# Kernel optimization log

Measured on AMD Instinct MI355X. Metric: run time of the kernel, lower is better.

Reference implementation:

```python
import jax, jax.numpy as jnp
import numpy as np

B, S, D = 2, 2048, 1024
H = 16
DH = D // H
FFN = 4096
EPS = 1e-5
SCALE = 1.0 / np.sqrt(DH).astype(np.float32)


def layer_norm(x, g, b):
    mu = jnp.mean(x, axis=-1, keepdims=True)
    var = jnp.mean(jnp.square(x - mu), axis=-1, keepdims=True)
    return (x - mu) * jax.lax.rsqrt(var + EPS) * g + b


def setup_inputs() -> dict:
    key = jax.random.key(0)
    ks = jax.random.split(key, 12)
    std = 0.02
    return {
        "x": jax.random.normal(ks[0], (B, S, D), dtype=jnp.float32),
        "mask": jax.random.randint(ks[1], (B, S), 0, 2, dtype=jnp.int32),
        "w_qkv": jax.random.normal(ks[2], (D, 3 * D), dtype=jnp.float32) * std,
        "w_out": jax.random.normal(ks[3], (D, D), dtype=jnp.float32) * std,
        "b_out": jnp.zeros((D,), dtype=jnp.float32),
        "g1": jnp.ones((D,), dtype=jnp.float32),
        "be1": jnp.zeros((D,), dtype=jnp.float32),
        "g2": jnp.ones((D,), dtype=jnp.float32),
        "be2": jnp.zeros((D,), dtype=jnp.float32),
        "w1": jax.random.normal(ks[4], (D, FFN), dtype=jnp.float32) * std,
        "b1": jnp.zeros((FFN,), dtype=jnp.float32),
        "w2": jax.random.normal(ks[5], (FFN, D), dtype=jnp.float32) * std,
        "b2": jnp.zeros((D,), dtype=jnp.float32),
    }


def reference(x, mask, w_qkv, w_out, b_out, g1, be1, g2, be2, w1, b1, w2, b2):
    # --- pre-norm self-attention ---
    h = layer_norm(x, g1, be1)                              # [B,S,D]
    qkv = (h @ w_qkv).reshape(B, S, 3, H, DH)               # [B,S,3,H,Dh]
    q, k, v = [jnp.transpose(qkv[:, :, i], (0, 2, 1, 3)) for i in range(3)]  # [B,H,S,Dh]
    scores = jnp.einsum("bhqd,bhkd->bhqk", q, k) * SCALE    # [B,H,S,S]
    key_mask = (mask != 0)[:, None, None, :]                # [B,1,1,S]
    scores = jnp.where(key_mask, scores, -1e9)
    attn = jax.nn.softmax(scores, axis=-1)
    out = jnp.einsum("bhqk,bhkd->bhqd", attn, v)            # [B,H,S,Dh]
    out = jnp.transpose(out, (0, 2, 1, 3)).reshape(B, S, D)
    x = x + (out @ w_out + b_out)
    # --- pre-norm FFN ---
    h2 = layer_norm(x, g2, be2)
    ffn = jax.nn.relu(h2 @ w1 + b1) @ w2 + b2
    return x + ffn
```

## Files before the change

### kernel.cpp

```cpp
#include <hip/hip_runtime.h>

typedef unsigned short u16;
typedef __bf16 bf16x8 __attribute__((ext_vector_type(8)));
typedef float f32x4 __attribute__((ext_vector_type(4)));

typedef __attribute__((address_space(1))) const void* as1cv;
typedef __attribute__((address_space(3))) void* as3v;

__device__ __forceinline__ u16 f2bf(float f) {
  union { float f; unsigned u; } v;
  v.f = f;
  unsigned r = (v.u + 0x7fffu + ((v.u >> 16) & 1u)) >> 16;
  return (u16)r;
}

__device__ __forceinline__ unsigned cvtpk(float lo, float hi) {
  unsigned r;
  asm("v_cvt_pk_bf16_f32 %0, %1, %2" : "=v"(r) : "v"(lo), "v"(hi));
  return r;
}

__device__ __forceinline__ void gload16(const void* g, void* l) {
  __builtin_amdgcn_global_load_lds((as1cv)g, (as3v)l, 16, 0, 0);
}

__global__ __launch_bounds__(256)
void ln_kernel(const float* __restrict__ x, const float* __restrict__ g,
               const float* __restrict__ be, u16* __restrict__ out) {
  __shared__ float red[8];
  const int row = blockIdx.x;
  const int tid = threadIdx.x;
  const float4 v = ((const float4*)(x + (size_t)row * 1024))[tid];
  float s = v.x + v.y + v.z + v.w;
#pragma unroll
  for (int off = 1; off < 64; off <<= 1) s += __shfl_xor(s, off, 64);
  const int wv = tid >> 6, lane = tid & 63;
  if (lane == 0) red[wv] = s;
  __syncthreads();
  s = red[0] + red[1] + red[2] + red[3];
  const float mu = s * (1.0f / 1024.0f);
  const float d0 = v.x - mu, d1 = v.y - mu, d2 = v.z - mu, d3 = v.w - mu;
  float q = d0 * d0 + d1 * d1 + d2 * d2 + d3 * d3;
#pragma unroll
  for (int off = 1; off < 64; off <<= 1) q += __shfl_xor(q, off, 64);
  if (lane == 0) red[4 + wv] = q;
  __syncthreads();
  q = red[4] + red[5] + red[6] + red[7];
  const float inv = rsqrtf(q * (1.0f / 1024.0f) + 1e-5f);
  const float4 gv = ((const float4*)g)[tid];
  const float4 bv = ((const float4*)be)[tid];
  unsigned p0 = (unsigned)f2bf(d0 * inv * gv.x + bv.x) |
                ((unsigned)f2bf(d1 * inv * gv.y + bv.y) << 16);
  unsigned p1 = (unsigned)f2bf(d2 * inv * gv.z + bv.z) |
                ((unsigned)f2bf(d3 * inv * gv.w + bv.w) << 16);
  uint2 o; o.x = p0; o.y = p1;
  *(uint2*)(out + (size_t)row * 1024 + tid * 4) = o;
}

__global__ __launch_bounds__(256)
void transpose_all(const float* __restrict__ i0, u16* __restrict__ o0,
                   const float* __restrict__ i1, u16* __restrict__ o1,
                   const float* __restrict__ i2, u16* __restrict__ o2,
                   const float* __restrict__ i3, u16* __restrict__ o3) {
  __shared__ float t[32][33];
  int id = blockIdx.x;
  const float* in; u16* out; int K, N, nx;
  if (id < 3072)      { in = i0; out = o0; K = 1024; N = 3072; nx = 96; }
  else if (id < 4096) { id -= 3072; in = i1; out = o1; K = 1024; N = 1024; nx = 32; }
  else if (id < 8192) { id -= 4096; in = i2; out = o2; K = 1024; N = 4096; nx = 128; }
  else                { id -= 8192; in = i3; out = o3; K = 4096; N = 1024; nx = 32; }
  const int n0 = (id % nx) * 32, k0 = (id / nx) * 32;
  const int tx = threadIdx.x & 31, ty = threadIdx.x >> 5;
  for (int r = ty; r < 32; r += 8)
    t[r][tx] = in[(size_t)(k0 + r) * N + n0 + tx];
  __syncthreads();
  for (int r = ty; r < 32; r += 8)
    out[(size_t)(n0 + r) * K + k0 + tx] = f2bf(t[tx][r]);
}

template<int BIAS, int RELU, int RES, int MODE, int NSPLIT>
__global__ __launch_bounds__(256, 2)
void gemm_bt(const u16* __restrict__ A, const u16* __restrict__ Bt,
             const float* __restrict__ bias, const float* __restrict__ res,
             void* __restrict__ C, u16* __restrict__ vt,
             int M, int N, int K, int kChunk) {
  __shared__ u16 As[4][4096];
  __shared__ u16 Bs[4][4096];
  const int tid = threadIdx.x;
  const int wv = tid >> 6, lane = tid & 63;
  const int z = (NSPLIT > 1) ? (int)(blockIdx.x % NSPLIT) : 0;
  const int bm = (int)(blockIdx.x / NSPLIT) * 128;
  const int bn = blockIdx.y * 128;
  const int wr = wv >> 1, wc = wv & 1;
  const int l16 = lane & 15, lh = lane >> 4;

  const int ssk = ((lane & 3) ^ ((lane >> 3) & 3)) << 3;
  const int rdk = (lh ^ ((l16 >> 1) & 3)) << 3;

  f32x4 acc[4][4] = {};

  const int kb = z * kChunk;
  const u16* Ag = A + (size_t)(bm + wv * 16 + (lane >> 2)) * K + kb + ssk;
  const u16* Bg = Bt + (size_t)(bn + wv * 16 + (lane >> 2)) * K + kb + ssk;

#define STG_A(buf, ko)  do { \
    gload16(Ag + (ko), &As[buf][wv * 512]); \
    gload16(Ag + (size_t)64 * K + (ko), &As[buf][2048 + wv * 512]); } while (0)
#define STG_B(buf, ko)  do { \
    gload16(Bg + (ko), &Bs[buf][wv * 512]); \
    gload16(Bg + (size_t)64 * K + (ko), &Bs[buf][2048 + wv * 512]); } while (0)

  const int nst = kChunk >> 5;
  STG_A(0, 0); STG_B(0, 0);
  if (nst > 1) { STG_A(1, 32); STG_B(1, 32); }
  if (nst > 2) { STG_A(2, 64); STG_B(2, 64); }

  for (int t = 0; t < nst; ++t) {
    const int cur = t & 3;
    const int rem = nst - t;
    if (rem >= 3)      asm volatile("s_waitcnt vmcnt(8)" ::: "memory");
    else if (rem == 2) asm volatile("s_waitcnt vmcnt(4)" ::: "memory");
    else               asm volatile("s_waitcnt vmcnt(0)" ::: "memory");
    __builtin_amdgcn_s_barrier();
    asm volatile("" ::: "memory");
    const int nxb = (t + 3) & 3;
    bf16x8 af[4], bfv[4];
#pragma unroll
    for (int i = 0; i < 4; i++)
      af[i] = *(const bf16x8*)&As[cur][(wr * 64 + i * 16 + l16) * 32 + rdk];
#pragma unroll
    for (int j = 0; j < 2; j++)
      bfv[j] = *(const bf16x8*)&Bs[cur][(wc * 64 + j * 16 + l16) * 32 + rdk];
    if (t + 3 < nst) STG_A(nxb, (t + 3) * 32);
    __builtin_amdgcn_s_setprio(1);
#pragma unroll
    for (int i = 0; i < 4; i++)
#pragma unroll
      for (int j = 0; j < 2; j++)
        acc[i][j] = __builtin_amdgcn_mfma_f32_16x16x32_bf16(af[i], bfv[j], acc[i][j], 0, 0, 0);
    __builtin_amdgcn_s_setprio(0);
#pragma unroll
    for (int j = 2; j < 4; j++)
      bfv[j] = *(const bf16x8*)&Bs[cur][(wc * 64 + j * 16 + l16) * 32 + rdk];
    if (t + 3 < nst) STG_B(nxb, (t + 3) * 32);
    __builtin_amdgcn_s_setprio(1);
#pragma unroll
    for (int i = 0; i < 4; i++)
#pragma unroll
      for (int j = 2; j < 4; j++)
        acc[i][j] = __builtin_amdgcn_mfma_f32_16x16x32_bf16(af[i], bfv[j], acc[i][j], 0, 0, 0);
    __builtin_amdgcn_s_setprio(0);
  }
#undef STG_A
#undef STG_B

#pragma unroll
  for (int i = 0; i < 4; i++) {
#pragma unroll
    for (int j = 0; j < 4; j++) {
      const int col = bn + wc * 64 + j * 16 + l16;
      const float bv = (BIAS && z == 0) ? bias[col] : 0.0f;
      if (MODE == 3 && bn >= 2048) {
        const int cc = col - 2048, h = cc >> 6, d = cc & 63;
        const int row0 = bm + wr * 64 + i * 16 + (lane >> 4) * 4;
        const int bb = row0 >> 11, kv0 = row0 & 2047;
        const int p0 = (kv0 & 32) | (((kv0 >> 2) & 3) << 3) | (((kv0 >> 4) & 1) << 2);
        uint2 o;
        o.x = (unsigned)f2bf(acc[i][j][0]) | ((unsigned)f2bf(acc[i][j][1]) << 16);
        o.y = (unsigned)f2bf(acc[i][j][2]) | ((unsigned)f2bf(acc[i][j][3]) << 16);
        *(uint2*)(vt + ((size_t)(bb * 16 + h) * 64 + d) * 2048 + (kv0 & ~63) + p0) = o;
      } else {
#pragma unroll
        for (int r = 0; r < 4; r++) {
          const int row = bm + wr * 64 + i * 16 + (lane >> 4) * 4 + r;
          float v = acc[i][j][r] + bv;
          if (RELU) v = fmaxf(v, 0.0f);
          if (RES) v += res[(size_t)row * N + col];
          if (MODE == 2)       atomicAdd((float*)C + (size_t)row * N + col, v);
          else if (MODE == 0)  ((float*)C)[(size_t)row * N + col] = v;
          else                 ((u16*)C)[(size_t)row * N + col] = f2bf(v);
        }
      }
    }
  }
}

template<int BIAS, int RELU, int MODE>
__global__ __launch_bounds__(512, 2)
void gemm256(const u16* __restrict__ A, const u16* __restrict__ Bt,
             const float* __restrict__ bias, u16* __restrict__ C,
             u16* __restrict__ vt, int M, int N, int K) {
  __shared__ u16 As[2][16384];
  __shared__ u16 Bs[2][16384];
  const int tid = threadIdx.x;
  const int wv = tid >> 6, lane = tid & 63;
  const int l16 = lane & 15, lh = lane >> 4;
  const int wm = wv >> 2, wn = wv & 3;
  const int bm = blockIdx.x * 256, bn = blockIdx.y * 256;

  const int koff = ((lane & 7) ^ ((lane >> 3) & 7)) << 3;
  const int ka0 = ((lh ^ (l16 & 7)) << 3);
  const int ka1 = (((4 + lh) ^ (l16 & 7)) << 3);

  f32x4 acc[8][4] = {};

  const u16* Ag = A + (size_t)(bm + wv * 8 + (lane >> 3)) * K + koff;
  const u16* Bg = Bt + (size_t)(bn + wv * 8 + (lane >> 3)) * K + koff;

#define STAGE256(buf, ko)                                                  \
  do {                                                                     \
    _Pragma("unroll")                                                      \
    for (int j = 0; j < 4; ++j) {                                          \
      gload16(Ag + (size_t)(j * 64) * K + (ko), &As[buf][j * 4096 + wv * 512]); \
      gload16(Bg + (size_t)(j * 64) * K + (ko), &Bs[buf][j * 4096 + wv * 512]); \
    }                                                                      \
  } while (0)

  const int nt = K >> 6;
  STAGE256(0, 0);
  if (nt > 1) STAGE256(1, 64);

  for (int t = 0; t < nt; ++t) {
    const int cur = t & 1;
    if (t + 1 < nt) asm volatile("s_waitcnt vmcnt(8)" ::: "memory");
    else            asm volatile("s_waitcnt vmcnt(0)" ::: "memory");
    __builtin_amdgcn_s_barrier();
    asm volatile("" ::: "memory");
#pragma unroll
    for (int kk = 0; kk < 2; ++kk) {
      const int ko = kk ? ka1 : ka0;
      bf16x8 af[8], bfv[4];
#pragma unroll
      for (int i = 0; i < 8; ++i)
        af[i] = *(const bf16x8*)&As[cur][(wm * 128 + i * 16 + l16) * 64 + ko];
#pragma unroll
      for (int n = 0; n < 4; ++n)
        bfv[n] = *(const bf16x8*)&Bs[cur][(wn * 64 + n * 16 + l16) * 64 + ko];
      __builtin_amdgcn_s_setprio(1);
#pragma unroll
      for (int i = 0; i < 8; ++i)
#pragma unroll
        for (int n = 0; n < 4; ++n)
          acc[i][n] = __builtin_amdgcn_mfma_f32_16x16x32_bf16(af[i], bfv[n], acc[i][n], 0, 0, 0);
      __builtin_amdgcn_s_setprio(0);
    }
    asm volatile("" ::: "memory");
    __builtin_amdgcn_s_barrier();
    asm volatile("" ::: "memory");
    if (t + 2 < nt) STAGE256(cur, (t + 2) * 64);
  }
#undef STAGE256

#pragma unroll
  for (int i = 0; i < 8; ++i)
#pragma unroll
    for (int n = 0; n < 4; ++n) {
      const int col = bn + wn * 64 + n * 16 + l16;
      const float bv = BIAS ? bias[col] : 0.0f;
      if (MODE == 3 && bn >= 2048) {
        const int cc = col - 2048, h = cc >> 6, d = cc & 63;
        const int row0 = bm + wm * 128 + i * 16 + lh * 4;
        const int bb = row0 >> 11, kv0 = row0 & 2047;
        const int p0 = (kv0 & 32) | (((kv0 >> 2) & 3) << 3) | (((kv0 >> 4) & 1) << 2);
        uint2 o;
        o.x = (unsigned)f2bf(acc[i][n][0]) | ((unsigned)f2bf(acc[i][n][1]) << 16);
        o.y = (unsigned)f2bf(acc[i][n][2]) | ((unsigned)f2bf(acc[i][n][3]) << 16);
        *(uint2*)(vt + ((size_t)(bb * 16 + h) * 64 + d) * 2048 + (kv0 & ~63) + p0) = o;
      } else {
#pragma unroll
        for (int r = 0; r < 4; ++r) {
          const int row = bm + wm * 128 + i * 16 + lh * 4 + r;
          float v = acc[i][n][r] + bv;
          if (RELU) v = fmaxf(v, 0.0f);
          C[(size_t)row * N + col] = f2bf(v);
        }
      }
    }
}

__global__ __launch_bounds__(256, 4)
void attn3(const u16* __restrict__ qkv, const u16* __restrict__ vT,
           const int* __restrict__ mask, u16* __restrict__ aout) {
  __shared__ u16 KsS[2][4096];
  __shared__ u16 VsS[2][4096];
  __shared__ float mbL[2048];

  const int tid = threadIdx.x;
  const int wv = tid >> 6, lane = tid & 63;
  const int l16 = lane & 15, lh = lane >> 4;
  const int bh = blockIdx.x, b = bh >> 4, h = bh & 15;
  const int q0 = blockIdx.y * 64 + wv * 16;

  {
    const int4* srcm = (const int4*)(mask + b * 2048);
    float4* dstm = (float4*)mbL;
#pragma unroll
    for (int u = 0; u < 2; ++u) {
      const int4 mv = srcm[tid + u * 256];
      float4 f;
      f.x = mv.x ? 0.f : -1.4426950408889634e9f;
      f.y = mv.y ? 0.f : -1.4426950408889634e9f;
      f.z = mv.z ? 0.f : -1.4426950408889634e9f;
      f.w = mv.w ? 0.f : -1.4426950408889634e9f;
      dstm[tid + u * 256] = f;
    }
  }

  bf16x8 qf[2];
#pragma unroll
  for (int c = 0; c < 2; ++c)
    qf[c] = *(const bf16x8*)(qkv + (size_t)(b * 2048 + q0 + l16) * 3072 + h * 64 + c * 32 + 8 * lh);

  const int rs = (l16 & 7) << 4;
  const int koff0 = ((16 * lh) ^ rs) >> 1;
  const int koff1 = ((64 + 16 * lh) ^ rs) >> 1;
  const int voff0 = koff0, voff1 = koff1;

  const int rl0 = wv * 8 + (lane >> 3);
  const int rl1 = 32 + wv * 8 + (lane >> 3);
  const int glog = (lane & 7) ^ ((lane >> 3) & 7);
  const u16* kg0 = qkv + (size_t)(b * 2048 + rl0) * 3072 + 1024 + h * 64 + 8 * glog;
  const u16* kg1 = qkv + (size_t)(b * 2048 + rl1) * 3072 + 1024 + h * 64 + 8 * glog;
  const u16* vg0 = vT + ((size_t)bh * 64 + rl0) * 2048 + 8 * glog;
  const u16* vg1 = vT + ((size_t)bh * 64 + rl1) * 2048 + 8 * glog;

  gload16(kg0, &KsS[0][wv * 512]);
  gload16(kg1, &KsS[0][2048 + wv * 512]);
  gload16(vg0, &VsS[0][wv * 512]);
  gload16(vg1, &VsS[0][2048 + wv * 512]);
  kg0 += 64 * 3072; kg1 += 64 * 3072; vg0 += 64; vg1 += 64;

  const float CL2 = 0.125f * 1.4426950408889634f;
  f32x4 lsum = {};
  f32x4 oT[4] = {};
  union U8 { unsigned u[4]; bf16x8 v; };
  U8 onesu;
  onesu.u[0] = onesu.u[1] = onesu.u[2] = onesu.u[3] = 0x3F803F80u;
  const bf16x8 ones = onesu.v;

  for (int t = 0; t < 32; ++t) {
    asm volatile("s_waitcnt vmcnt(0)" ::: "memory");
    __syncthreads();
    const int cur = t & 1;
    if (t + 1 < 32) {
      const int nx = cur ^ 1;
      gload16(kg0, &KsS[nx][wv * 512]);
      gload16(kg1, &KsS[nx][2048 + wv * 512]);
      gload16(vg0, &VsS[nx][wv * 512]);
      gload16(vg1, &VsS[nx][2048 + wv * 512]);
      kg0 += 64 * 3072; kg1 += 64 * 3072; vg0 += 64; vg1 += 64;
    }

    const u16* Kb = &KsS[cur][0];
    const u16* Vb = &VsS[cur][0];

    f32x4 mbc[4];
#pragma unroll
    for (int n = 0; n < 4; ++n)
      mbc[n] = *(const f32x4*)&mbL[t * 64 + n * 16 + 4 * lh];

    f32x4 s[4] = {};
    __builtin_amdgcn_s_setprio(1);
#pragma unroll
    for (int c = 0; c < 2; ++c) {
      const int ko = c ? koff1 : koff0;
      bf16x8 kf[4];
#pragma unroll
      for (int n = 0; n < 4; ++n)
        kf[n] = *(const bf16x8*)(Kb + (n * 16 + l16) * 64 + ko);
#pragma unroll
      for (int n = 0; n < 4; ++n)
        s[n] = __builtin_amdgcn_mfma_f32_16x16x32_bf16(kf[n], qf[c], s[n], 0, 0, 0);
    }
    __builtin_amdgcn_s_setprio(0);

#pragma unroll
    for (int n = 0; n < 4; ++n)
#pragma unroll
      for (int j = 0; j < 4; ++j)
        s[n][j] = __builtin_exp2f(fmaf(s[n][j], CL2, mbc[n][j]));

    U8 pa[2];
#pragma unroll
    for (int u = 0; u < 2; ++u) {
      pa[u].u[0] = cvtpk(s[2 * u][0], s[2 * u][1]);
      pa[u].u[1] = cvtpk(s[2 * u][2], s[2 * u][3]);
      pa[u].u[2] = cvtpk(s[2 * u + 1][0], s[2 * u + 1][1]);
      pa[u].u[3] = cvtpk(s[2 * u + 1][2], s[2 * u + 1][3]);
    }

    __builtin_amdgcn_s_setprio(1);
#pragma unroll
    for (int u = 0; u < 2; ++u) {
      const int vo = u ? voff1 : voff0;
      lsum = __builtin_amdgcn_mfma_f32_16x16x32_bf16(ones, pa[u].v, lsum, 0, 0, 0);
#pragma unroll
      for (int D = 0; D < 4; ++D) {
        const bf16x8 va = *(const bf16x8*)(Vb + (D * 16 + l16) * 64 + vo);
        oT[D] = __builtin_amdgcn_mfma_f32_16x16x32_bf16(va, pa[u].v, oT[D], 0, 0, 0);
      }
    }
    __builtin_amdgcn_s_setprio(0);
  }

  const float rr = 1.0f / lsum[0];
#pragma unroll
  for (int D = 0; D < 4; ++D) {
    uint2 o;
    o.x = cvtpk(oT[D][0] * rr, oT[D][1] * rr);
    o.y = cvtpk(oT[D][2] * rr, oT[D][3] * rr);
    *(uint2*)(aout + (size_t)(b * 2048 + q0 + l16) * 1024 + h * 64 + D * 16 + 4 * lh) = o;
  }
}

extern "C" void kernel_launch(void* const* d_in, const int* in_sizes, int n_in,
                              void* d_out, int out_size, void* d_ws, size_t ws_size,
                              hipStream_t stream) {
  (void)in_sizes; (void)n_in; (void)out_size; (void)ws_size;
  const float* x     = (const float*)d_in[0];
  const int*   mask  = (const int*)d_in[1];
  const float* w_qkv = (const float*)d_in[2];
  const float* w_out = (const float*)d_in[3];
  const float* b_out = (const float*)d_in[4];
  const float* g1    = (const float*)d_in[5];
  const float* be1   = (const float*)d_in[6];
  const float* g2    = (const float*)d_in[7];
  const float* be2   = (const float*)d_in[8];
  const float* w1    = (const float*)d_in[9];
  const float* b1    = (const float*)d_in[10];
  const float* w2    = (const float*)d_in[11];
  const float* b2    = (const float*)d_in[12];
  float* out = (float*)d_out;

  char* ws = (char*)d_ws;
  u16* hA    = (u16*)(ws);
  u16* wqkvT = (u16*)(ws + 8388608);
  u16* woutT = (u16*)(ws + 14680064);
  u16* w1T   = (u16*)(ws + 16777216);
  u16* w2T   = (u16*)(ws + 25165824);
  u16* qkv   = (u16*)(ws + 33554432);
  u16* ffn1  = (u16*)(ws + 33554432);
  u16* vTb   = (u16*)(ws + 67108864);
  u16* aout  = (u16*)(ws + 75497472);

  ln_kernel<<<4096, 256, 0, stream>>>(x, g1, be1, hA);
  transpose_all<<<12288, 256, 0, stream>>>(w_qkv, wqkvT, w_out, woutT, w1, w1T, w2, w2T);
  gemm256<0, 0, 3><<<dim3(16, 12), 512, 0, stream>>>(hA, wqkvT, nullptr, qkv, vTb, 4096, 3072, 1024);
  attn3<<<dim3(32, 32), 256, 0, stream>>>(qkv, vTb, mask, aout);
  gemm_bt<1, 0, 1, 0, 1><<<dim3(32, 8), 256, 0, stream>>>(aout, woutT, b_out, x, out, nullptr, 4096, 1024, 1024, 1024);
  ln_kernel<<<4096, 256, 0, stream>>>(out, g2, be2, hA);
  gemm256<1, 1, 1><<<dim3(16, 16), 512, 0, stream>>>(hA, w1T, b1, ffn1, nullptr, 4096, 4096, 1024);
  gemm_bt<1, 0, 0, 2, 2><<<dim3(64, 8), 256, 0, stream>>>(ffn1, w2T, b2, nullptr, out, nullptr, 4096, 1024, 4096, 2048);
}
```

Measured before the change: 246.9 us.

## Replace 128x128 gemm_bt with 128x64 tile GEMM and drop split-K atomics

The two N=1024 GEMMs (out-projection and FFN down-projection) now use a 128x64 tile kernel, which gives 512 blocks instead of 256. The FFN2 GEMM no longer uses 2-way split-K with atomicAdd. It runs the full K=4096 per block and adds the residual in place by reading and writing out. The intent is to fill the GPU better, remove atomic traffic, and allow 3 blocks per CU. The trade-off is less data reuse per tile and a longer serial K loop for FFN2.

```diff
diff --git a/kernel.cpp b/kernel.cpp
--- a/kernel.cpp
+++ b/kernel.cpp
@@ -78,108 +78,80 @@
     out[(size_t)(n0 + r) * K + k0 + tx] = f2bf(t[tx][r]);
 }
 
-template<int BIAS, int RELU, int RES, int MODE, int NSPLIT>
-__global__ __launch_bounds__(256, 2)
-void gemm_bt(const u16* __restrict__ A, const u16* __restrict__ Bt,
-             const float* __restrict__ bias, const float* __restrict__ res,
-             void* __restrict__ C, u16* __restrict__ vt,
-             int M, int N, int K, int kChunk) {
+__global__ __launch_bounds__(256, 3)
+void gemm64(const u16* __restrict__ A, const u16* __restrict__ Bt,
+            const float* __restrict__ bias, const float* __restrict__ res,
+            float* __restrict__ C, int M, int N, int K) {
   __shared__ u16 As[4][4096];
-  __shared__ u16 Bs[4][4096];
+  __shared__ u16 Bs[4][2048];
   const int tid = threadIdx.x;
   const int wv = tid >> 6, lane = tid & 63;
-  const int z = (NSPLIT > 1) ? (int)(blockIdx.x % NSPLIT) : 0;
-  const int bm = (int)(blockIdx.x / NSPLIT) * 128;
-  const int bn = blockIdx.y * 128;
+  const int bm = blockIdx.x * 128;
+  const int bn = blockIdx.y * 64;
   const int wr = wv >> 1, wc = wv & 1;
   const int l16 = lane & 15, lh = lane >> 4;
 
   const int ssk = ((lane & 3) ^ ((lane >> 3) & 3)) << 3;
   const int rdk = (lh ^ ((l16 >> 1) & 3)) << 3;
 
-  f32x4 acc[4][4] = {};
-
-  const int kb = z * kChunk;
-  const u16* Ag = A + (size_t)(bm + wv * 16 + (lane >> 2)) * K + kb + ssk;
-  const u16* Bg = Bt + (size_t)(bn + wv * 16 + (lane >> 2)) * K + kb + ssk;
-
-#define STG_A(buf, ko)  do { \
+  f32x4 acc[4][2] = {};
+
+  const u16* Ag = A + (size_t)(bm + wv * 16 + (lane >> 2)) * K + ssk;
+  const u16* Bg = Bt + (size_t)(bn + wv * 16 + (lane >> 2)) * K + ssk;
+
+#define STG_A64(buf, ko)  do { \
     gload16(Ag + (ko), &As[buf][wv * 512]); \
     gload16(Ag + (size_t)64 * K + (ko), &As[buf][2048 + wv * 512]); } while (0)
-#define STG_B(buf, ko)  do { \
-    gload16(Bg + (ko), &Bs[buf][wv * 512]); \
-    gload16(Bg + (size_t)64 * K + (ko), &Bs[buf][2048 + wv * 512]); } while (0)
-
-  const int nst = kChunk >> 5;
-  STG_A(0, 0); STG_B(0, 0);
-  if (nst > 1) { STG_A(1, 32); STG_B(1, 32); }
-  if (nst > 2) { STG_A(2, 64); STG_B(2, 64); }
+#define STG_B64(buf, ko)  do { \
+    gload16(Bg + (ko), &Bs[buf][wv * 512]); } while (0)
+
+  const int nst = K >> 5;
+  STG_A64(0, 0); STG_B64(0, 0);
+  STG_A64(1, 32); STG_B64(1, 32);
+  STG_A64(2, 64); STG_B64(2, 64);
 
   for (int t = 0; t < nst; ++t) {
     const int cur = t & 3;
     const int rem = nst - t;
-    if (rem >= 3)      asm volatile("s_waitcnt vmcnt(8)" ::: "memory");
-    else if (rem == 2) asm volatile("s_waitcnt vmcnt(4)" ::: "memory");
+    if (rem >= 3)      asm volatile("s_waitcnt vmcnt(6)" ::: "memory");
+    else if (rem == 2) asm volatile("s_waitcnt vmcnt(3)" ::: "memory");
     else               asm volatile("s_waitcnt vmcnt(0)" ::: "memory");
     __builtin_amdgcn_s_barrier();
     asm volatile("" ::: "memory");
     const int nxb = (t + 3) & 3;
-    bf16x8 af[4], bfv[4];
+    bf16x8 af[4], bfv[2];
 #pragma unroll
     for (int i = 0; i < 4; i++)
       af[i] = *(const bf16x8*)&As[cur][(wr * 64 + i * 16 + l16) * 32 + rdk];
-#pragma unroll
-    for (int j = 0; j < 2; j++)
-      bfv[j] = *(const bf16x8*)&Bs[cur][(wc * 64 + j * 16 + l16) * 32 + rdk];
-    if (t + 3 < nst) STG_A(nxb, (t + 3) * 32);
+    bfv[0] = *(const bf16x8*)&Bs[cur][(wc * 32 + l16) * 32 + rdk];
+    if (t + 3 < nst) STG_A64(nxb, (t + 3) * 32);
     __builtin_amdgcn_s_setprio(1);
 #pragma unroll
     for (int i = 0; i < 4; i++)
-#pragma unroll
-      for (int j = 0; j < 2; j++)
-        acc[i][j] = __builtin_amdgcn_mfma_f32_16x16x32_bf16(af[i], bfv[j], acc[i][j], 0, 0, 0);
+      acc[i][0] = __builtin_amdgcn_mfma_f32_16x16x32_bf16(af[i], bfv[0], acc[i][0], 0, 0, 0);
     __builtin_amdgcn_s_setprio(0);
-#pragma unroll
-    for (int j = 2; j < 4; j++)
-      bfv[j] = *(const bf16x8*)&Bs[cur][(wc * 64 + j * 16 + l16) * 32 + rdk];
-    if (t + 3 < nst) STG_B(nxb, (t + 3) * 32);
+    bfv[1] = *(const bf16x8*)&Bs[cur][(wc * 32 + 16 + l16) * 32 + rdk];
+    if (t + 3 < nst) STG_B64(nxb, (t + 3) * 32);
     __builtin_amdgcn_s_setprio(1);
 #pragma unroll
     for (int i = 0; i < 4; i++)
-#pragma unroll
-      for (int j = 2; j < 4; j++)
-        acc[i][j] = __builtin_amdgcn_mfma_f32_16x16x32_bf16(af[i], bfv[j], acc[i][j], 0, 0, 0);
+      acc[i][1] = __builtin_amdgcn_mfma_f32_16x16x32_bf16(af[i], bfv[1], acc[i][1], 0, 0, 0);
     __builtin_amdgcn_s_setprio(0);
   }
-#undef STG_A
-#undef STG_B
+#undef STG_A64
+#undef STG_B64
 
 #pragma unroll
   for (int i = 0; i < 4; i++) {
 #pragma unroll
-    for (int j = 0; j < 4; j++) {
-      const int col = bn + wc * 64 + j * 16 + l16;
-      const float bv = (BIAS && z == 0) ? bias[col] : 0.0f;
-      if (MODE == 3 && bn >= 2048) {
-        const int cc = col - 2048, h = cc >> 6, d = cc & 63;
-        const int row0 = bm + wr * 64 + i * 16 + (lane >> 4) * 4;
-        const int bb = row0 >> 11, kv0 = row0 & 2047;
-        const int p0 = (kv0 & 32) | (((kv0 >> 2) & 3) << 3) | (((kv0 >> 4) & 1) << 2);
-        uint2 o;
-        o.x = (unsigned)f2bf(acc[i][j][0]) | ((unsigned)f2bf(acc[i][j][1]) << 16);
-        o.y = (unsigned)f2bf(acc[i][j][2]) | ((unsigned)f2bf(acc[i][j][3]) << 16);
-        *(uint2*)(vt + ((size_t)(bb * 16 + h) * 64 + d) * 2048 + (kv0 & ~63) + p0) = o;
-      } else {
-#pragma unroll
-        for (int r = 0; r < 4; r++) {
-          const int row = bm + wr * 64 + i * 16 + (lane >> 4) * 4 + r;
-          float v = acc[i][j][r] + bv;
-          if (RELU) v = fmaxf(v, 0.0f);
-          if (RES) v += res[(size_t)row * N + col];
-          if (MODE == 2)       atomicAdd((float*)C + (size_t)row * N + col, v);
-          else if (MODE == 0)  ((float*)C)[(size_t)row * N + col] = v;
-          else                 ((u16*)C)[(size_t)row * N + col] = f2bf(v);
-        }
+    for (int j = 0; j < 2; j++) {
+      const int col = bn + wc * 32 + j * 16 + l16;
+      const float bv = bias[col];
+#pragma unroll
+      for (int r = 0; r < 4; r++) {
+        const int row = bm + wr * 64 + i * 16 + lh * 4 + r;
+        const float v = acc[i][j][r] + bv + res[(size_t)row * N + col];
+        C[(size_t)row * N + col] = v;
       }
     }
   }
@@ -447,8 +419,8 @@
   transpose_all<<<12288, 256, 0, stream>>>(w_qkv, wqkvT, w_out, woutT, w1, w1T, w2, w2T);
   gemm256<0, 0, 3><<<dim3(16, 12), 512, 0, stream>>>(hA, wqkvT, nullptr, qkv, vTb, 4096, 3072, 1024);
   attn3<<<dim3(32, 32), 256, 0, stream>>>(qkv, vTb, mask, aout);
-  gemm_bt<1, 0, 1, 0, 1><<<dim3(32, 8), 256, 0, stream>>>(aout, woutT, b_out, x, out, nullptr, 4096, 1024, 1024, 1024);
+  gemm64<<<dim3(32, 16), 256, 0, stream>>>(aout, woutT, b_out, x, out, 4096, 1024, 1024);
   ln_kernel<<<4096, 256, 0, stream>>>(out, g2, be2, hA);
   gemm256<1, 1, 1><<<dim3(16, 16), 512, 0, stream>>>(hA, w1T, b1, ffn1, nullptr, 4096, 4096, 1024);
-  gemm_bt<1, 0, 0, 2, 2><<<dim3(64, 8), 256, 0, stream>>>(ffn1, w2T, b2, nullptr, out, nullptr, 4096, 1024, 4096, 2048);
-}
+  gemm64<<<dim3(32, 16), 256, 0, stream>>>(ffn1, w2T, b2, out, out, 4096, 1024, 4096);
+}
```

Result: faster. 240.5 us (-2.6%).
